# Performance work log

Hardware: AMD Instinct MI355X
Metric: run time of the kernel (lower is better)

Reference implementation:

```python
import jax, jax.numpy as jnp
import numpy as np

B, T_ENC, U = 8, 200, 100
VOCAB, ENC_DIM, PRED_DIM, EMBED_DIM = 1024, 512, 512, 128


def setup_inputs() -> dict:
    key = jax.random.key(0)
    ks = jax.random.split(key, 13)
    n = lambda k, shape, fan_in: (jax.random.normal(k, shape, jnp.float32) / np.sqrt(fan_in)).astype(jnp.float32)
    return {
        "enc_out": jax.random.normal(ks[0], (B, T_ENC, ENC_DIM), jnp.float32),
        "targets": jax.random.randint(ks[1], (B, U), 0, VOCAB, jnp.int32),
        "target_len": jnp.full((B,), U, jnp.int32),
        # params
        "emb_table": n(ks[2], (VOCAB + 1, EMBED_DIM), 1.0),
        "W_ih": n(ks[3], (4 * PRED_DIM, EMBED_DIM), EMBED_DIM),
        "W_hh": n(ks[4], (4 * PRED_DIM, PRED_DIM), PRED_DIM),
        "b_ih": jnp.zeros((4 * PRED_DIM,), jnp.float32),
        "b_hh": jnp.zeros((4 * PRED_DIM,), jnp.float32),
        "W_enc": n(ks[5], (PRED_DIM, ENC_DIM), ENC_DIM),
        "b_enc": jnp.zeros((PRED_DIM,), jnp.float32),
        "W_pred": n(ks[6], (PRED_DIM, PRED_DIM), PRED_DIM),
        "b_pred": jnp.zeros((PRED_DIM,), jnp.float32),
        "W_joint": n(ks[7], (VOCAB + 1, PRED_DIM), PRED_DIM),
        "b_joint": jnp.zeros((VOCAB + 1,), jnp.float32),
    }


def reference(enc_out, targets, target_len, emb_table, W_ih, W_hh, b_ih, b_hh,
              W_enc, b_enc, W_pred, b_pred, W_joint, b_joint):
    # targets_with_blank: prepend blank_id = vocab_size
    blank_id = emb_table.shape[0] - 1
    Bsz = targets.shape[0]
    tw = jnp.concatenate([jnp.full((Bsz, 1), blank_id, targets.dtype), targets], axis=1)
    emb = emb_table[tw]  # (B, U+1, E)

    P = W_hh.shape[1]
    h0 = jnp.zeros((Bsz, P), emb.dtype)

    def lstm_step(carry, x_t):
        h, c = carry
        gates = x_t @ W_ih.T + b_ih + h @ W_hh.T + b_hh  # (B, 4P)
        i, f, g, o = jnp.split(gates, 4, axis=-1)  # PyTorch LSTMCell gate order
        i, f, o = jax.nn.sigmoid(i), jax.nn.sigmoid(f), jax.nn.sigmoid(o)
        c = f * c + i * jnp.tanh(g)
        h = o * jnp.tanh(c)
        return (h, c), h

    _, pred = jax.lax.scan(lstm_step, (h0, h0), jnp.swapaxes(emb, 0, 1))
    pred = jnp.swapaxes(pred, 0, 1)  # (B, U+1, P)

    f_enc = enc_out @ W_enc.T + b_enc   # (B, T, P)
    f_pred = pred @ W_pred.T + b_pred   # (B, U+1, P)
    joint = jnp.tanh(f_enc[:, :, None, :] + f_pred[:, None, :, :])  # (B, T, U+1, P)
    logits = joint @ W_joint.T + b_joint  # (B, T, U+1, V+1)
    return logits
```

## Files before the change

### kernel.cpp

```cpp
#include <hip/hip_runtime.h>
#include <stdint.h>
#include <stddef.h>

#define BB 8
#define TENC 200
#define UU 100
#define UP1 101
#define VP1 1025
#define ED 128
#define PD 512
#define LSTM_NWG 64
#define MTOT 161600
#define MB_  20200

typedef __attribute__((ext_vector_type(8))) unsigned short ushort8;
typedef __attribute__((ext_vector_type(8))) __bf16 bf16x8;
typedef __attribute__((ext_vector_type(4))) float f32x4;

__device__ __forceinline__ float bf2f(unsigned short u){
  unsigned int x = ((unsigned int)u) << 16;
  return __builtin_bit_cast(float, x);
}
__device__ __forceinline__ unsigned short f2bf(float f){
  unsigned int x = __builtin_bit_cast(unsigned int, f);
  unsigned int r = (x + 0x7fffu + ((x >> 16) & 1u)) >> 16;
  return (unsigned short)r;
}
__device__ __forceinline__ float tanh_fast(float x){
  float e = __expf(2.0f * x);
  return 1.0f - 2.0f / (e + 1.0f);
}
__device__ __forceinline__ float sigm(float x){
  return 1.0f / (1.0f + __expf(-x));
}
__device__ __forceinline__ void gload_lds16(const unsigned short* gsrc, unsigned short* ldst){
  __builtin_amdgcn_global_load_lds((const __attribute__((address_space(1))) void*)gsrc,
                                   (__attribute__((address_space(3))) void*)ldst, 16, 0, 0);
}

__global__ __launch_bounds__(256) void k_cvt_bf16(const float* __restrict__ src,
                                                  unsigned short* __restrict__ dst, int n){
  int i = blockIdx.x * 256 + threadIdx.x;
  if (i < n) dst[i] = f2bf(src[i]);
}

__global__ __launch_bounds__(256) void k_xgate(
    const float* __restrict__ emb, const int* __restrict__ targets,
    const float* __restrict__ W_ih, const float* __restrict__ b_ih,
    const float* __restrict__ b_hh, float* __restrict__ xg)
{
  __shared__ float e_s[BB * ED];
  const int u  = blockIdx.x >> 2;
  const int jq = blockIdx.x & 3;
  const int tid = threadIdx.x;
  for (int idx = tid; idx < BB * ED; idx += 256){
    int b = idx >> 7, e = idx & 127;
    int tok = (u == 0) ? 1024 : targets[b * UU + (u - 1)];
    e_s[idx] = emb[(size_t)tok * ED + e];
  }
  __syncthreads();
  float acc[2][BB];
  #pragma unroll
  for (int r = 0; r < 2; r++)
    #pragma unroll
    for (int b = 0; b < BB; b++) acc[r][b] = 0.0f;
  const int j0 = jq * 512 + tid;
  const float* w0p = W_ih + (size_t)j0 * ED;
  const float* w1p = W_ih + (size_t)(j0 + 256) * ED;
  for (int e = 0; e < ED; e++){
    float w0 = w0p[e], w1 = w1p[e];
    #pragma unroll
    for (int b = 0; b < BB; b++){
      float ev = e_s[b * ED + e];
      acc[0][b] = fmaf(ev, w0, acc[0][b]);
      acc[1][b] = fmaf(ev, w1, acc[1][b]);
    }
  }
  #pragma unroll
  for (int r = 0; r < 2; r++){
    int j = j0 + r * 256;
    float bias = b_ih[j] + b_hh[j];
    #pragma unroll
    for (int b = 0; b < BB; b++)
      xg[((size_t)b * UP1 + u) * 2048 + j] = acc[r][b] + bias;
  }
}

__global__ __launch_bounds__(256) void k_lstm_all(
    const float* __restrict__ xg, const float* __restrict__ W_hh,
    float* __restrict__ pred, float* __restrict__ hb, unsigned int* __restrict__ seq)
{
  __shared__ float h_s[8][520];
  __shared__ float red[32 * 257];
  __shared__ float gates_s[32][9];
  const int tid = threadIdx.x;
  const int wg  = blockIdx.x;
  const int p0  = wg * 8;
  const int jg = tid >> 5, kc = tid & 31;
  const float* wrow[4];
  #pragma unroll
  for (int r = 0; r < 4; r++){
    int jl = jg * 4 + r;
    int grow = (jl >> 3) * PD + p0 + (jl & 7);
    wrow[r] = W_hh + (size_t)grow * PD;
  }
  float c_reg = 0.0f;
  for (int u = 0; u < UP1; u++){
    float xi = 0.f, xf = 0.f, xgv = 0.f, xo = 0.f;
    if (tid < 64){
      int pl = tid >> 3, b = tid & 7;
      const float* xr = xg + ((size_t)(b * UP1 + u)) * 2048;
      int p = p0 + pl;
      xi = xr[p]; xf = xr[512 + p]; xgv = xr[1024 + p]; xo = xr[1536 + p];
    }
    if (u > 0){
      if (tid < 64){
        while (1){
          unsigned int v = __hip_atomic_load(&seq[tid * 16], __ATOMIC_RELAXED, __HIP_MEMORY_SCOPE_AGENT);
          if (__all(v >= (unsigned int)u)) break;
          __builtin_amdgcn_s_sleep(1);
        }
      }
      __syncthreads();
      const float* hsrc = hb + ((u - 1) & 1) * 4096;
      float tmp[16];
      #pragma unroll
      for (int j = 0; j < 16; j++)
        tmp[j] = __hip_atomic_load(hsrc + tid + 256 * j,
                                   __ATOMIC_RELAXED, __HIP_MEMORY_SCOPE_AGENT);
      #pragma unroll
      for (int j = 0; j < 16; j++){
        int i = tid + 256 * j;
        h_s[i >> 9][i & 511] = tmp[j];
      }
    } else {
      for (int i = tid; i < 8 * PD; i += 256) h_s[i >> 9][i & 511] = 0.0f;
    }
    __syncthreads();
    float acc[4][BB];
    #pragma unroll
    for (int r = 0; r < 4; r++)
      #pragma unroll
      for (int b = 0; b < BB; b++) acc[r][b] = 0.0f;
    for (int i = 0; i < 16; i++){
      int k = kc + 32 * i;
      float hv[BB];
      #pragma unroll
      for (int b = 0; b < BB; b++) hv[b] = h_s[b][k];
      #pragma unroll
      for (int r = 0; r < 4; r++){
        float wv = wrow[r][k];
        #pragma unroll
        for (int b = 0; b < BB; b++) acc[r][b] = fmaf(hv[b], wv, acc[r][b]);
      }
    }
    #pragma unroll
    for (int r = 0; r < 4; r++)
      #pragma unroll
      for (int b = 0; b < BB; b++)
        red[kc * 257 + jg * 32 + r * 8 + b] = acc[r][b];
    __syncthreads();
    {
      int jl = tid >> 3, b = tid & 7;
      float s = 0.0f;
      #pragma unroll
      for (int kk = 0; kk < 32; kk++)
        s += red[kk * 257 + (jl >> 2) * 32 + (jl & 3) * 8 + b];
      gates_s[jl][b] = s;
    }
    __syncthreads();
    if (tid < 64){
      int pl = tid >> 3, b2 = tid & 7;
      int p = p0 + pl;
      float gi = gates_s[0  + pl][b2] + xi;
      float gf = gates_s[8  + pl][b2] + xf;
      float gg = gates_s[16 + pl][b2] + xgv;
      float go = gates_s[24 + pl][b2] + xo;
      float iv = sigm(gi), fv = sigm(gf), ov = sigm(go);
      c_reg = fv * c_reg + iv * tanh_fast(gg);
      float hval = ov * tanh_fast(c_reg);
      __hip_atomic_store(hb + (u & 1) * 4096 + b2 * 512 + p, hval,
                         __ATOMIC_RELAXED, __HIP_MEMORY_SCOPE_AGENT);
      pred[((size_t)(b2 * UP1 + u)) * PD + p] = hval;
    }
    if (u < UP1 - 1 && tid == 0){
      asm volatile("s_waitcnt vmcnt(0)" ::: "memory");
      __hip_atomic_store(&seq[wg * 16], (unsigned int)(u + 1),
                         __ATOMIC_RELAXED, __HIP_MEMORY_SCOPE_AGENT);
    }
  }
}

__global__ __launch_bounds__(256) void k_gemm_bias_bf16(
    const float* __restrict__ A, const float* __restrict__ W,
    const float* __restrict__ bias, unsigned short* __restrict__ out, int M)
{
  __shared__ float a_s[16][68];
  __shared__ float b_s[16][68];
  const int m0 = blockIdx.x * 64, n0 = blockIdx.y * 64;
  const int tid = threadIdx.x;
  const int tx = tid & 15, ty = tid >> 4;
  float acc[4][4];
  #pragma unroll
  for (int i2 = 0; i2 < 4; i2++)
    #pragma unroll
    for (int j2 = 0; j2 < 4; j2++) acc[i2][j2] = 0.0f;
  for (int k0 = 0; k0 < 512; k0 += 16){
    int mm = tid >> 2, k4 = (tid & 3) * 4;
    int row = m0 + mm; if (row >= M) row = M - 1;
    float4 av = *(const float4*)(A + (size_t)row * 512 + k0 + k4);
    a_s[k4 + 0][mm] = av.x; a_s[k4 + 1][mm] = av.y;
    a_s[k4 + 2][mm] = av.z; a_s[k4 + 3][mm] = av.w;
    float4 bv = *(const float4*)(W + (size_t)(n0 + mm) * 512 + k0 + k4);
    b_s[k4 + 0][mm] = bv.x; b_s[k4 + 1][mm] = bv.y;
    b_s[k4 + 2][mm] = bv.z; b_s[k4 + 3][mm] = bv.w;
    __syncthreads();
    #pragma unroll
    for (int k = 0; k < 16; k++){
      float4 a4 = *(const float4*)&a_s[k][ty * 4];
      float4 b4 = *(const float4*)&b_s[k][tx * 4];
      float aa[4] = {a4.x, a4.y, a4.z, a4.w};
      float bb[4] = {b4.x, b4.y, b4.z, b4.w};
      #pragma unroll
      for (int i2 = 0; i2 < 4; i2++)
        #pragma unroll
        for (int j2 = 0; j2 < 4; j2++)
          acc[i2][j2] = fmaf(aa[i2], bb[j2], acc[i2][j2]);
    }
    __syncthreads();
  }
  #pragma unroll
  for (int i2 = 0; i2 < 4; i2++){
    int m = m0 + ty * 4 + i2;
    if (m < M){
      #pragma unroll
      for (int j2 = 0; j2 < 4; j2++){
        int n = n0 + tx * 4 + j2;
        out[(size_t)m * 512 + n] = f2bf(acc[i2][j2] + bias[n]);
      }
    }
  }
}

__global__ __launch_bounds__(256) void k_tanhA(
    const unsigned short* __restrict__ fe, const unsigned short* __restrict__ fp,
    const unsigned short* __restrict__ wj, const float* __restrict__ bj,
    unsigned short* __restrict__ Aout, float* __restrict__ out,
    int m_base, int M_cnt)
{
  const int tid = threadIdx.x;
  const int mlocal = blockIdx.x * 4 + (tid >> 6);
  if (mlocal >= M_cnt) return;
  const int l = tid & 63;
  const int m = m_base + mlocal;
  const int q = m / 101;
  const int u = m - q * 101;
  const int b = q / 200;
  ushort8 f8 = *(const ushort8*)(fe + (size_t)q * 512 + l * 8);
  ushort8 p8 = *(const ushort8*)(fp + (size_t)(b * 101 + u) * 512 + l * 8);
  ushort8 w8 = *(const ushort8*)(wj + (size_t)1024 * 512 + l * 8);
  ushort8 a;
  float s = 0.0f;
  #pragma unroll
  for (int e = 0; e < 8; e++){
    float v = tanh_fast(bf2f(f8[e]) + bf2f(p8[e]));
    a[e] = f2bf(v);
    s += v * bf2f(w8[e]);
  }
  *(ushort8*)(Aout + (size_t)mlocal * 512 + l * 8) = a;
  #pragma unroll
  for (int off = 1; off < 64; off <<= 1) s += __shfl_xor(s, off);
  if (l == 0) out[(size_t)m * VP1 + 1024] = s + bj[1024];
}

__global__ __launch_bounds__(256, 4) void k_joint7s(
    const unsigned short* __restrict__ A, const unsigned short* __restrict__ wj,
    const float* __restrict__ bj, float* __restrict__ out,
    int m_base, int M_cnt, int nmt)
{
  __shared__ unsigned short A_s[2][128 * 32];
  __shared__ unsigned short B_s[2][128 * 32];
  const int bid = blockIdx.x;
  const int mt  = (bid >> 6) * 8 + (bid & 7);
  if (mt >= nmt) return;
  const int m0 = mt * 128;
  const int n0 = ((bid >> 3) & 7) * 128;
  const int tid = threadIdx.x;
  const int w = tid >> 6, l = tid & 63;
  const int l15 = l & 15, lg = l >> 4;
  const int wr = w >> 1, wc = w & 1;

  auto stage = [&](int buf, int kc){
    #pragma unroll
    for (int i = 0; i < 2; i++){
      int sbase = i * 256 + w * 64;
      int slot  = sbase + l;
      int r  = slot >> 2;
      int cs = slot & 3;
      int col8 = cs ^ ((r >> 1) & 3);
      int ra = m0 + r; if (ra >= M_cnt) ra = M_cnt - 1;
      gload_lds16(A + (size_t)ra * 512 + kc * 32 + col8 * 8,
                  (unsigned short*)A_s[buf] + (size_t)sbase * 8);
      gload_lds16(wj + (size_t)(n0 + r) * 512 + kc * 32 + col8 * 8,
                  (unsigned short*)B_s[buf] + (size_t)sbase * 8);
    }
  };

  stage(0, 0);
  __syncthreads();

  f32x4 acc[4][4];
  #pragma unroll
  for (int fr = 0; fr < 4; fr++)
    #pragma unroll
    for (int fc = 0; fc < 4; fc++)
      acc[fr][fc] = (f32x4){0.f, 0.f, 0.f, 0.f};

  for (int kc = 0; kc < 16; kc++){
    const int buf = kc & 1;
    if (kc < 15) stage(buf ^ 1, kc + 1);
    bf16x8 afr[4], bfr[4];
    #pragma unroll
    for (int f = 0; f < 4; f++){
      int ra = wr * 64 + f * 16 + l15;
      int bya = ra * 64 + ((lg ^ ((ra >> 1) & 3)) * 16);
      afr[f] = __builtin_bit_cast(bf16x8, *(const ushort8*)((const char*)A_s[buf] + bya));
      int rb = wc * 64 + f * 16 + l15;
      int byb = rb * 64 + ((lg ^ ((rb >> 1) & 3)) * 16);
      bfr[f] = __builtin_bit_cast(bf16x8, *(const ushort8*)((const char*)B_s[buf] + byb));
    }
    #pragma unroll
    for (int fr = 0; fr < 4; fr++)
      #pragma unroll
      for (int fc = 0; fc < 4; fc++)
        acc[fr][fc] = __builtin_amdgcn_mfma_f32_16x16x32_bf16(bfr[fc], afr[fr], acc[fr][fc], 0, 0, 0);
    __syncthreads();
  }

  #pragma unroll
  for (int fr = 0; fr < 4; fr++){
    int mloc = m0 + wr * 64 + fr * 16 + l15;
    if (mloc < M_cnt){
      float* orow = out + (size_t)(m_base + mloc) * VP1;
      #pragma unroll
      for (int fc = 0; fc < 4; fc++){
        int col = n0 + wc * 64 + fc * 16 + lg * 4;
        float4 bv = *(const float4*)(bj + col);
        f32x4 v = acc[fr][fc];
        float4 st = {v[0] + bv.x, v[1] + bv.y, v[2] + bv.z, v[3] + bv.w};
        *(float4*)(orow + col) = st;
      }
    }
  }
}

extern "C" void kernel_launch(void* const* d_in, const int* in_sizes, int n_in,
                              void* d_out, int out_size, void* d_ws, size_t ws_size,
                              hipStream_t stream) {
  const float* enc_out = (const float*)d_in[0];
  const int*   targets = (const int*)d_in[1];
  const float* emb     = (const float*)d_in[3];
  const float* W_ih    = (const float*)d_in[4];
  const float* W_hh    = (const float*)d_in[5];
  const float* b_ih    = (const float*)d_in[6];
  const float* b_hh    = (const float*)d_in[7];
  const float* W_enc   = (const float*)d_in[8];
  const float* b_enc   = (const float*)d_in[9];
  const float* W_pred  = (const float*)d_in[10];
  const float* b_pred  = (const float*)d_in[11];
  const float* W_joint = (const float*)d_in[12];
  const float* b_joint = (const float*)d_in[13];
  float* out = (float*)d_out;

  char* ws = (char*)d_ws;
  float* xg            = (float*)(ws + 0);
  float* pred          = (float*)(ws + 6619136);
  unsigned short* feb  = (unsigned short*)(ws + 8273920);
  unsigned short* fpb  = (unsigned short*)(ws + 9912320);
  unsigned short* wjb  = (unsigned short*)(ws + 10739712);
  float* hb            = (float*)(ws + 11789312);
  unsigned int* seq    = (unsigned int*)(ws + 11822080);
  unsigned short* Abuf = (unsigned short*)(ws + 11827200);
  const size_t FULL_NEED  = 11827200 + (size_t)MTOT * 512 * 2;
  const size_t BATCH_NEED = 11827200 + (size_t)MB_  * 512 * 2;

  (void)hipMemsetAsync(seq, 0, 4096, stream);
  hipLaunchKernelGGL(k_cvt_bf16, dim3((VP1 * 512 + 255) / 256), dim3(256), 0, stream,
                     W_joint, wjb, VP1 * 512);
  hipLaunchKernelGGL(k_xgate, dim3(404), dim3(256), 0, stream,
                     emb, targets, W_ih, b_ih, b_hh, xg);
  hipLaunchKernelGGL(k_gemm_bias_bf16, dim3(25, 8), dim3(256), 0, stream,
                     enc_out, W_enc, b_enc, feb, 1600);
  hipLaunchKernelGGL(k_lstm_all, dim3(LSTM_NWG), dim3(256), 0, stream,
                     xg, W_hh, pred, hb, seq);
  hipLaunchKernelGGL(k_gemm_bias_bf16, dim3(13, 8), dim3(256), 0, stream,
                     pred, W_pred, b_pred, fpb, 808);

  if (ws_size >= FULL_NEED){
    const int nmt = 1263;
    const int grid = 8 * 8 * ((nmt + 7) / 8);
    hipLaunchKernelGGL(k_tanhA, dim3(MTOT / 4), dim3(256), 0, stream,
                       feb, fpb, wjb, b_joint, Abuf, out, 0, MTOT);
    hipLaunchKernelGGL(k_joint7s, dim3(grid), dim3(256), 0, stream,
                       Abuf, wjb, b_joint, out, 0, MTOT, nmt);
  } else if (ws_size >= BATCH_NEED){
    const int nmt = 158;
    const int grid = 8 * 8 * ((nmt + 7) / 8);
    for (int b = 0; b < 8; b++){
      hipLaunchKernelGGL(k_tanhA, dim3(MB_ / 4), dim3(256), 0, stream,
                         feb, fpb, wjb, b_joint, Abuf, out, b * MB_, MB_);
      hipLaunchKernelGGL(k_joint7s, dim3(grid), dim3(256), 0, stream,
                         Abuf, wjb, b_joint, out, b * MB_, MB_, nmt);
    }
  } else {
    const int nmt = 40;
    const int grid = 8 * 8 * ((nmt + 7) / 8);
    for (int c = 0; c < 32; c++){
      hipLaunchKernelGGL(k_tanhA, dim3(5050 / 2, 1), dim3(256), 0, stream,
                         feb, fpb, wjb, b_joint, Abuf, out, c * 5050, 5050);
      hipLaunchKernelGGL(k_joint7s, dim3(grid), dim3(256), 0, stream,
                         Abuf, wjb, b_joint, out, c * 5050, 5050, nmt);
    }
  }
}
```

Baseline: 870.2 us.

## Replace LSTM sequence-flag barrier with tagged 64-bit hidden-state values

The persistent LSTM kernel used to wait on per-workgroup sequence counters, then issue a separate load of the hidden state. Each hidden value is now stored as a 64-bit word that carries its step number, so consumers poll the data itself until every tag matches. This removes the separate flag store, its vmcnt wait and one round trip per step. In exchange every thread polls 16 doubled-width loads and the hidden-state buffer is twice as large.

```diff
diff --git a/kernel.cpp b/kernel.cpp
--- a/kernel.cpp
+++ b/kernel.cpp
@@ -88,7 +88,7 @@
 
 __global__ __launch_bounds__(256) void k_lstm_all(
     const float* __restrict__ xg, const float* __restrict__ W_hh,
-    float* __restrict__ pred, float* __restrict__ hb, unsigned int* __restrict__ seq)
+    float* __restrict__ pred, unsigned long long* __restrict__ hbt)
 {
   __shared__ float h_s[8][520];
   __shared__ float red[32 * 257];
@@ -114,24 +114,24 @@
       xi = xr[p]; xf = xr[512 + p]; xgv = xr[1024 + p]; xo = xr[1536 + p];
     }
     if (u > 0){
-      if (tid < 64){
-        while (1){
-          unsigned int v = __hip_atomic_load(&seq[tid * 16], __ATOMIC_RELAXED, __HIP_MEMORY_SCOPE_AGENT);
-          if (__all(v >= (unsigned int)u)) break;
-          __builtin_amdgcn_s_sleep(1);
-        }
+      const unsigned long long* hsrc = hbt + ((u - 1) & 1) * 4096;
+      unsigned long long v[16];
+      while (1){
+        #pragma unroll
+        for (int j = 0; j < 16; j++)
+          v[j] = __hip_atomic_load(hsrc + tid + 256 * j,
+                                   __ATOMIC_RELAXED, __HIP_MEMORY_SCOPE_AGENT);
+        bool ok = true;
+        #pragma unroll
+        for (int j = 0; j < 16; j++)
+          ok &= ((unsigned int)(v[j] >> 32) == (unsigned int)u);
+        if (ok) break;
+        __builtin_amdgcn_s_sleep(1);
       }
-      __syncthreads();
-      const float* hsrc = hb + ((u - 1) & 1) * 4096;
-      float tmp[16];
-      #pragma unroll
-      for (int j = 0; j < 16; j++)
-        tmp[j] = __hip_atomic_load(hsrc + tid + 256 * j,
-                                   __ATOMIC_RELAXED, __HIP_MEMORY_SCOPE_AGENT);
       #pragma unroll
       for (int j = 0; j < 16; j++){
         int i = tid + 256 * j;
-        h_s[i >> 9][i & 511] = tmp[j];
+        h_s[i >> 9][i & 511] = __builtin_bit_cast(float, (unsigned int)(v[j] & 0xffffffffu));
       }
     } else {
       for (int i = tid; i < 8 * PD; i += 256) h_s[i >> 9][i & 511] = 0.0f;
@@ -179,14 +179,11 @@
       float iv = sigm(gi), fv = sigm(gf), ov = sigm(go);
       c_reg = fv * c_reg + iv * tanh_fast(gg);
       float hval = ov * tanh_fast(c_reg);
-      __hip_atomic_store(hb + (u & 1) * 4096 + b2 * 512 + p, hval,
+      unsigned long long pk = ((unsigned long long)(unsigned int)(u + 1) << 32)
+                            | (unsigned long long)__builtin_bit_cast(unsigned int, hval);
+      __hip_atomic_store(hbt + (u & 1) * 4096 + b2 * 512 + p, pk,
                          __ATOMIC_RELAXED, __HIP_MEMORY_SCOPE_AGENT);
       pred[((size_t)(b2 * UP1 + u)) * PD + p] = hval;
-    }
-    if (u < UP1 - 1 && tid == 0){
-      asm volatile("s_waitcnt vmcnt(0)" ::: "memory");
-      __hip_atomic_store(&seq[wg * 16], (unsigned int)(u + 1),
-                         __ATOMIC_RELAXED, __HIP_MEMORY_SCOPE_AGENT);
     }
   }
 }
@@ -378,13 +375,12 @@
   unsigned short* feb  = (unsigned short*)(ws + 8273920);
   unsigned short* fpb  = (unsigned short*)(ws + 9912320);
   unsigned short* wjb  = (unsigned short*)(ws + 10739712);
-  float* hb            = (float*)(ws + 11789312);
-  unsigned int* seq    = (unsigned int*)(ws + 11822080);
-  unsigned short* Abuf = (unsigned short*)(ws + 11827200);
-  const size_t FULL_NEED  = 11827200 + (size_t)MTOT * 512 * 2;
-  const size_t BATCH_NEED = 11827200 + (size_t)MB_  * 512 * 2;
-
-  (void)hipMemsetAsync(seq, 0, 4096, stream);
+  unsigned long long* hbt = (unsigned long long*)(ws + 11789312);
+  unsigned short* Abuf = (unsigned short*)(ws + 11854848);
+  const size_t FULL_NEED  = 11854848 + (size_t)MTOT * 512 * 2;
+  const size_t BATCH_NEED = 11854848 + (size_t)MB_  * 512 * 2;
+
+  (void)hipMemsetAsync(hbt, 0, 65536, stream);
   hipLaunchKernelGGL(k_cvt_bf16, dim3((VP1 * 512 + 255) / 256), dim3(256), 0, stream,
                      W_joint, wjb, VP1 * 512);
   hipLaunchKernelGGL(k_xgate, dim3(404), dim3(256), 0, stream,
@@ -392,7 +388,7 @@
   hipLaunchKernelGGL(k_gemm_bias_bf16, dim3(25, 8), dim3(256), 0, stream,
                      enc_out, W_enc, b_enc, feb, 1600);
   hipLaunchKernelGGL(k_lstm_all, dim3(LSTM_NWG), dim3(256), 0, stream,
-                     xg, W_hh, pred, hb, seq);
+                     xg, W_hh, pred, hbt);
   hipLaunchKernelGGL(k_gemm_bias_bf16, dim3(13, 8), dim3(256), 0, stream,
                      pred, W_pred, b_pred, fpb, 808);
 
```

Result: slower. 939.6 us (+8.0%).
